# Kernel tuning notes

Hardware: AMD Instinct MI355X
Metric: run time of the kernel (lower is better)

The kernel has to match this reference:

```python
import jax, jax.numpy as jnp
import numpy as np

N_HEAD = 12
HEAD_DIM = 64
EPS = 1e-6
ROPE_BASE = 10000.0


def rms_norm(x, w):
    x32 = x.astype(jnp.float32)
    var = jnp.mean(x32 * x32, axis=-1, keepdims=True)
    xn = x32 * jax.lax.rsqrt(var + EPS)
    return w * xn.astype(x.dtype)


def rotate_half(x):
    x1, x2 = jnp.split(x, 2, axis=-1)
    return jnp.concatenate((-x2, x1), axis=-1)


def rope_cos_sin(seq_len, dtype):
    inv_freq = 1.0 / (ROPE_BASE ** (jnp.arange(0, HEAD_DIM, 2, dtype=jnp.float32) / HEAD_DIM))
    pos = jnp.arange(seq_len, dtype=jnp.float32)
    freqs = pos[:, None] * inv_freq[None, :]          # [S, HEAD_DIM//2]
    emb = jnp.concatenate((freqs, freqs), axis=-1)    # [S, HEAD_DIM]
    # shape [1, 1, S, HEAD_DIM] (batch, head, seq, dim) after unsqueeze_dim=1
    return emb[None, None].astype(dtype), None  # placeholder, see below


def setup_inputs() -> dict:
    key = jax.random.key(0)
    ks = jax.random.split(key, 9)
    B, S, D, F = 1, 4096, 768, 2048
    s = 0.02
    return {
        "hidden_states": jax.random.normal(ks[0], (B, S, D), jnp.float32),
        "w_q": jax.random.normal(ks[1], (D, D), jnp.float32) * s,
        "w_k": jax.random.normal(ks[2], (D, D), jnp.float32) * s,
        "w_v": jax.random.normal(ks[3], (D, D), jnp.float32) * s,
        "w_o": jax.random.normal(ks[4], (D, D), jnp.float32) * s,
        "w_gate": jax.random.normal(ks[5], (D, F), jnp.float32) * s,
        "w_up": jax.random.normal(ks[6], (D, F), jnp.float32) * s,
        "w_down": jax.random.normal(ks[7], (F, D), jnp.float32) * s,
        "w_norm1": jnp.ones((D,), jnp.float32),
        "w_norm2": jnp.ones((D,), jnp.float32),
    }


def attention(x, w_q, w_k, w_v, w_o):
    B, S, D = x.shape
    scale = HEAD_DIM ** -0.5
    # project and split heads: [B, H, S, hd]
    q = (x @ w_q).reshape(B, S, N_HEAD, HEAD_DIM).transpose(0, 2, 1, 3)
    k = (x @ w_k).reshape(B, S, N_HEAD, HEAD_DIM).transpose(0, 2, 1, 3)
    v = (x @ w_v).reshape(B, S, N_HEAD, HEAD_DIM).transpose(0, 2, 1, 3)
    # rotary embedding (position_ids = arange(S))
    inv_freq = 1.0 / (ROPE_BASE ** (jnp.arange(0, HEAD_DIM, 2, dtype=jnp.float32) / HEAD_DIM))
    pos = jnp.arange(S, dtype=jnp.float32)
    freqs = pos[:, None] * inv_freq[None, :]
    emb = jnp.concatenate((freqs, freqs), axis=-1)          # [S, hd]
    cos = jnp.cos(emb).astype(x.dtype)[None, None]          # [1,1,S,hd]
    sin = jnp.sin(emb).astype(x.dtype)[None, None]
    q = q * cos + rotate_half(q) * sin
    k = k * cos + rotate_half(k) * sin
    # eager attention with causal mask (materialized, as in the original)
    scores = jnp.einsum("bhqd,bhkd->bhqk", q, k) * scale
    causal = jnp.triu(jnp.ones((S, S), dtype=bool), k=1)
    scores = jnp.where(causal, jnp.finfo(scores.dtype).min, scores)
    attn = jax.nn.softmax(scores.astype(jnp.float32), axis=-1).astype(q.dtype)
    out = jnp.einsum("bhqk,bhkd->bhqd", attn, v)
    out = out.transpose(0, 2, 1, 3).reshape(B, S, D)
    return out @ w_o


def reference(hidden_states, w_q, w_k, w_v, w_o, w_gate, w_up, w_down, w_norm1, w_norm2):
    x = hidden_states
    h = x + attention(rms_norm(x, w_norm1), w_q, w_k, w_v, w_o)
    y = rms_norm(h, w_norm2)
    ffn = (jax.nn.silu(y @ w_gate) * (y @ w_up)) @ w_down
    return h + ffn
```

## Files before the change

### kernel.cpp

```cpp
#include <hip/hip_runtime.h>
#include <hip/hip_bf16.h>

typedef __attribute__((ext_vector_type(8))) short s8v;
typedef __attribute__((ext_vector_type(4))) float f4v;
typedef __attribute__((ext_vector_type(16))) float f16v;
typedef __attribute__((ext_vector_type(4))) unsigned u4v;

typedef __attribute__((address_space(1))) const void as1_void;
typedef __attribute__((address_space(3))) void as3_void;

__device__ __forceinline__ void gl16(const void* g, void* l) {
  __builtin_amdgcn_global_load_lds((as1_void*)g, (as3_void*)l, 16, 0, 0);
}

__device__ __forceinline__ float b2f(int u) {
  union { float f; unsigned i; } c; c.i = ((unsigned)(u & 0xFFFF)) << 16; return c.f;
}
__device__ __forceinline__ unsigned short f2b(float f) {
  union { float f; unsigned i; } c; c.f = f;
  unsigned r = c.i + 0x7FFFu + ((c.i >> 16) & 1u);
  return (unsigned short)(r >> 16);
}
__device__ __forceinline__ unsigned pk2(float lo, float hi) {
  unsigned u;
  asm("v_cvt_pk_bf16_f32 %0, %1, %2" : "=v"(u) : "v"(lo), "v"(hi));
  return u;
}

#define MFMA16(a, b, c) __builtin_amdgcn_mfma_f32_16x16x32_bf16((a), (b), (c), 0, 0, 0)
#define MFMA32(a, b, c) __builtin_amdgcn_mfma_f32_32x32x16_bf16((a), (b), (c), 0, 0, 0)

struct Seg { const float* src; unsigned short* dst; int K; int N; int nbn; int nblocks; int mode; };
struct PrepArgs { Seg seg[9]; float* ct; float* st; const float* wn1; };

__global__ __launch_bounds__(256) void prep_k(PrepArgs a) {
  int b = blockIdx.x, si = 0;
  while (si < 8 && b >= a.seg[si].nblocks) { b -= a.seg[si].nblocks; ++si; }
  const Seg s = a.seg[si];
  const int tid = threadIdx.x;
  if (s.mode == 3) {
    const int t = b * 256 + tid;
    const int sq = t >> 5, d = t & 31;
    const float inv = powf(10000.0f, -(float)d * (1.0f / 32.0f));
    const float ang = (float)sq * inv;
    a.ct[t] = cosf(ang);
    a.st[t] = sinf(ang);
    return;
  }
  if (s.mode == 4) {
    const float* xr = s.src + (size_t)b * 768;
    float v0 = xr[tid], v1 = xr[tid + 256], v2 = xr[tid + 512];
    float ss = v0 * v0 + v1 * v1 + v2 * v2;
#pragma unroll
    for (int m = 1; m < 64; m <<= 1) ss += __shfl_xor(ss, m, 64);
    __shared__ float sred[4];
    if ((tid & 63) == 0) sred[tid >> 6] = ss;
    __syncthreads();
    const float tot = sred[0] + sred[1] + sred[2] + sred[3];
    const float rn = rsqrtf(tot * (1.0f / 768.0f) + 1e-6f);
    unsigned short* orow = s.dst + (size_t)b * 768;
    orow[tid]       = f2b(v0 * rn * a.wn1[tid]);
    orow[tid + 256] = f2b(v1 * rn * a.wn1[tid + 256]);
    orow[tid + 512] = f2b(v2 * rn * a.wn1[tid + 512]);
    return;
  }
  __shared__ float tile[32][33];
  const int tx = tid & 31, ty = tid >> 5;
  const int bn = b % s.nbn, bk = b / s.nbn;
#pragma unroll
  for (int i = 0; i < 32; i += 8)
    tile[ty + i][tx] = s.src[(size_t)(bk * 32 + ty + i) * s.N + bn * 32 + tx];
  __syncthreads();
#pragma unroll
  for (int i = 0; i < 32; i += 8) {
    int row;
    if (s.mode == 0)      row = bn * 32 + ty + i;
    else                  row = bn * 64 + (s.mode == 2 ? 32 : 0) + ty + i;
    s.dst[(size_t)row * s.K + bk * 32 + tx] = f2b(tile[tx][ty + i]);
  }
}

__global__ __launch_bounds__(256) void rmsnorm_k(const float* __restrict__ x,
    const float* __restrict__ w, unsigned short* __restrict__ out) {
  const int row = blockIdx.x, tid = threadIdx.x;
  const float* xr = x + (size_t)row * 768;
  float v0 = xr[tid], v1 = xr[tid + 256], v2 = xr[tid + 512];
  float ss = v0 * v0 + v1 * v1 + v2 * v2;
#pragma unroll
  for (int m = 1; m < 64; m <<= 1) ss += __shfl_xor(ss, m, 64);
  __shared__ float sred[4];
  if ((tid & 63) == 0) sred[tid >> 6] = ss;
  __syncthreads();
  const float tot = sred[0] + sred[1] + sred[2] + sred[3];
  const float rn = rsqrtf(tot * (1.0f / 768.0f) + 1e-6f);
  unsigned short* orow = out + (size_t)row * 768;
  orow[tid]       = f2b(v0 * rn * w[tid]);
  orow[tid + 256] = f2b(v1 * rn * w[tid + 256]);
  orow[tid + 512] = f2b(v2 * rn * w[tid + 512]);
}

template <int EPI, int BN>
__global__ __launch_bounds__(256) void gemm_bt(const unsigned short* __restrict__ A,
    const unsigned short* __restrict__ Bt, unsigned short* __restrict__ Cb,
    float* __restrict__ Cf, const float* __restrict__ R, int K, int ldc,
    const float* __restrict__ ct, const float* __restrict__ st) {
  constexpr int ABYTES = 128 * 32 * 2;
  constexpr int BBYTES = BN * 32 * 2;
  constexpr int MR = (BN == 128) ? 4 : 2;
  __shared__ unsigned short As[3 * 128 * 32];
  __shared__ unsigned short Bs[3 * BN * 32];
  const int tid = threadIdx.x;
  const int lane = tid & 63, wid = tid >> 6;
  const int wrow = (BN == 128) ? (wid >> 1) * 64 : wid * 32;
  const int wcol = (BN == 128) ? (wid & 1) * 64 : 0;
  const int l15 = lane & 15, l4 = lane >> 4;
  const int bm = blockIdx.y, bn = blockIdx.x;

  f4v acc[MR][4] = {};

  const int o0 = tid * 16, o1 = tid * 16 + 4096;
  const int r0 = o0 >> 6, c0 = o0 & 63;
  const int r1 = o1 >> 6, c1 = o1 & 63;
  const size_t ldab = (size_t)K * 2;
  const char* Abyte = (const char*)A;
  const char* Bbyte = (const char*)Bt;
  const size_t a0 = (size_t)(bm * 128 + r0) * ldab + c0;
  const size_t a1 = (size_t)(bm * 128 + r1) * ldab + c1;
  const size_t b0 = (size_t)(bn * BN + r0) * ldab + c0;
  const size_t b1 = (size_t)(bn * BN + r1) * ldab + c1;
  char* AsB = (char*)As;
  char* BsB = (char*)Bs;
  const int uoff = wid << 10;

#define STAGEK(I, SL) do { const size_t kb = (size_t)(I) * 64;                 \
    char* Aw = AsB + (SL) * ABYTES;                                            \
    char* Bw = BsB + (SL) * BBYTES;                                            \
    gl16(Abyte + a0 + kb, Aw + uoff);                                          \
    gl16(Abyte + a1 + kb, Aw + uoff + 4096);                                   \
    gl16(Bbyte + b0 + kb, Bw + uoff);                                          \
    if constexpr (BN == 128) gl16(Bbyte + b1 + kb, Bw + uoff + 4096); } while (0)

  const int NI = K >> 5;
  STAGEK(0, 0);
  STAGEK(1, 1);
  int sel = 0, nsl = 2;

  for (int i = 0; i < NI; ++i) {
    if (i < NI - 1) {
      if constexpr (BN == 128) asm volatile("s_waitcnt vmcnt(4)" ::: "memory");
      else                     asm volatile("s_waitcnt vmcnt(3)" ::: "memory");
    } else {
      asm volatile("s_waitcnt vmcnt(0)" ::: "memory");
    }
    __builtin_amdgcn_s_barrier();
    __builtin_amdgcn_sched_barrier(0);
    if (i + 2 < NI) STAGEK(i + 2, nsl);
    const char* Ar = AsB + sel * ABYTES;
    const char* Br = BsB + sel * BBYTES;
    s8v af[MR], bf[4];
#pragma unroll
    for (int m = 0; m < MR; ++m)
      af[m] = *(const s8v*)(Ar + (wrow + m * 16 + l15) * 64 + l4 * 16);
#pragma unroll
    for (int n = 0; n < 4; ++n)
      bf[n] = *(const s8v*)(Br + (wcol + n * 16 + l15) * 64 + l4 * 16);
    __builtin_amdgcn_s_setprio(1);
#pragma unroll
    for (int m = 0; m < MR; ++m)
#pragma unroll
      for (int n = 0; n < 4; ++n) acc[m][n] = MFMA16(af[m], bf[n], acc[m][n]);
    __builtin_amdgcn_s_setprio(0);
    sel = (sel == 2) ? 0 : sel + 1;
    nsl = (nsl == 2) ? 0 : nsl + 1;
  }
#undef STAGEK

  const int row0 = bm * 128 + wrow;
  const int col0 = bn * BN + wcol;

  if (EPI == 2 && bn < 12) {
#pragma unroll
    for (int m = 0; m < MR; ++m)
#pragma unroll
      for (int r = 0; r < 4; ++r) {
        const int row = row0 + m * 16 + l4 * 4 + r;
#pragma unroll
        for (int n = 0; n < 2; ++n) {
          const int d = n * 16 + l15;
          const float c  = ct[row * 32 + d];
          const float sn = st[row * 32 + d];
          const float aa = acc[m][n][r], bb = acc[m][n + 2][r];
          acc[m][n][r]     = aa * c - bb * sn;
          acc[m][n + 2][r] = bb * c + aa * sn;
        }
      }
  }
  if (EPI == 2 && bn < 6) {
    const float QSC = 0.18033688011112042f;
#pragma unroll
    for (int m = 0; m < MR; ++m)
#pragma unroll
      for (int n = 0; n < 4; ++n)
#pragma unroll
        for (int r = 0; r < 4; ++r) acc[m][n][r] *= QSC;
  }

  if (EPI == 3) {
    const int wcx = wcol >> 6;
    const int colb = (bn * 2 + wcx) * 32;
#pragma unroll
    for (int m = 0; m < MR; ++m)
#pragma unroll
      for (int n = 0; n < 2; ++n)
#pragma unroll
        for (int r = 0; r < 4; ++r) {
          const int row = row0 + m * 16 + l4 * 4 + r;
          const float g = acc[m][n][r], u = acc[m][n + 2][r];
          const float val = g * u / (1.0f + __expf(-g));
          Cb[(size_t)row * 2048 + colb + n * 16 + l15] = f2b(val);
        }
    return;
  }

#pragma unroll
  for (int m = 0; m < MR; ++m)
#pragma unroll
    for (int n = 0; n < 4; ++n)
#pragma unroll
      for (int r = 0; r < 4; ++r) {
        const int row = row0 + m * 16 + l4 * 4 + r;
        const int col = col0 + n * 16 + l15;
        const float v = acc[m][n][r];
        if (EPI == 1) {
          Cf[(size_t)row * ldc + col] = v + R[(size_t)row * ldc + col];
        } else {
          Cb[(size_t)row * ldc + col] = f2b(v);
        }
      }
}

__global__ __launch_bounds__(256, 4) void flash_k(const unsigned short* __restrict__ qkv,
    uint2* __restrict__ Opart, float* __restrict__ ml) {
  const int kh = blockIdx.x, p = blockIdx.y, h = blockIdx.z;
  const int qbA = 63 - p;
  const int tid = threadIdx.x;
  const int wv = tid >> 6, lane = tid & 63;
  const int l31 = lane & 31, h8 = lane >> 5;
  const int myqb = (wv & 1) ? p : qbA;
  const int qrel = (wv >> 1) * 32 + l31;
  const int q_abs = myqb * 64 + qrel;

  __shared__ unsigned short Ks[2][64 * 72];
  __shared__ unsigned short Vt[2][64 * 72];

  const unsigned short* qp = qkv + h * 64;
  const unsigned short* kp = qkv + 768 + h * 64;
  const unsigned short* vp = qkv + 1536 + h * 64;

  s8v qf[4];
#pragma unroll
  for (int cc = 0; cc < 4; ++cc)
    qf[cc] = *(const s8v*)(qp + (size_t)q_abs * 2304 + cc * 16 + h8 * 8);

  f16v o0 = {}, o1 = {};
  float lp = 0.f;

  const int krow = tid >> 3, kc = (tid & 7) * 8;
  const int vj = tid & 31, vd0 = (tid >> 5) * 8;

  s8v ka, kb, va, vb;
#define LOADT(T) do { const size_t k0n = (size_t)(T) * 64;                    \
    ka = *(const s8v*)(kp + (k0n + krow) * 2304 + kc);                        \
    kb = *(const s8v*)(kp + (k0n + krow + 32) * 2304 + kc);                   \
    va = *(const s8v*)(vp + (k0n + 2 * vj) * 2304 + vd0);                     \
    vb = *(const s8v*)(vp + (k0n + 2 * vj + 1) * 2304 + vd0); } while (0)
#define WRITET(BUF) do {                                                      \
    *(s8v*)(Ks[BUF] + krow * 72 + kc) = ka;                                   \
    *(s8v*)(Ks[BUF] + (krow + 32) * 72 + kc) = kb;                            \
    unsigned* vtw = (unsigned*)(Vt[BUF] + (size_t)vd0 * 72 + 2 * vj);         \
    _Pragma("unroll")                                                         \
    for (int i = 0; i < 8; ++i)                                               \
      vtw[i * 36] = ((unsigned)(unsigned short)va[i]) |                       \
                    (((unsigned)(unsigned short)vb[i]) << 16); } while (0)

  LOADT(kh);
  WRITET(0);
  if (kh + 2 <= qbA) LOADT(kh + 2);
  __syncthreads();

  for (int t = kh; t <= qbA; t += 2) {
    const int cur = (t >> 1) & 1;
    if (t <= myqb) {
      f16v s0 = {}, s1 = {};
      __builtin_amdgcn_s_setprio(1);
#pragma unroll
      for (int cc = 0; cc < 4; ++cc) {
        const s8v kf0 = *(const s8v*)(Ks[cur] + l31 * 72 + cc * 16 + h8 * 8);
        const s8v kf1 = *(const s8v*)(Ks[cur] + (32 + l31) * 72 + cc * 16 + h8 * 8);
        s0 = MFMA32(kf0, qf[cc], s0);
        s1 = MFMA32(kf1, qf[cc], s1);
      }
      __builtin_amdgcn_s_setprio(0);
      if (t == myqb) {
#pragma unroll
        for (int rr = 0; rr < 16; ++rr) {
          const int koff = (rr & 3) + 8 * (rr >> 2) + 4 * h8;
          if (koff > qrel) s0[rr] = -1e30f;
          if (koff + 32 > qrel) s1[rr] = -1e30f;
        }
      }
#pragma unroll
      for (int rr = 0; rr < 16; ++rr) {
        s0[rr] = exp2f(s0[rr]);
        s1[rr] = exp2f(s1[rr]);
      }
      float sm[8];
#pragma unroll
      for (int i = 0; i < 8; ++i) sm[i] = (s0[i] + s0[i + 8]) + (s1[i] + s1[i + 8]);
#pragma unroll
      for (int i = 0; i < 4; ++i) sm[i] += sm[i + 4];
      lp += (sm[0] + sm[1]) + (sm[2] + sm[3]);

      unsigned pk0[8], pk1[8];
#pragma unroll
      for (int g = 0; g < 4; ++g)
#pragma unroll
        for (int j = 0; j < 2; ++j) {
          pk0[g * 2 + j] = pk2(s0[g * 4 + 2 * j], s0[g * 4 + 2 * j + 1]);
          pk1[g * 2 + j] = pk2(s1[g * 4 + 2 * j], s1[g * 4 + 2 * j + 1]);
        }
      __builtin_amdgcn_s_setprio(1);
#pragma unroll
      for (int cc = 0; cc < 4; ++cc) {
        const int g0 = (cc & 1) * 2, g1 = g0 + 1;
        const unsigned pA0 = (cc & 2) ? pk1[g0 * 2 + 0] : pk0[g0 * 2 + 0];
        const unsigned pA1 = (cc & 2) ? pk1[g0 * 2 + 1] : pk0[g0 * 2 + 1];
        const unsigned pB0 = (cc & 2) ? pk1[g1 * 2 + 0] : pk0[g1 * 2 + 0];
        const unsigned pB1 = (cc & 2) ? pk1[g1 * 2 + 1] : pk0[g1 * 2 + 1];
        const unsigned t00 = __shfl_xor((int)pA0, 32);
        const unsigned t01 = __shfl_xor((int)pA1, 32);
        const unsigned t10 = __shfl_xor((int)pB0, 32);
        const unsigned t11 = __shfl_xor((int)pB1, 32);
        union { u4v u; s8v s; } pf;
        pf.u[0] = h8 ? t10 : pA0;
        pf.u[1] = h8 ? t11 : pA1;
        pf.u[2] = h8 ? pB0 : t00;
        pf.u[3] = h8 ? pB1 : t01;
        const s8v vf0 = *(const s8v*)(Vt[cur] + l31 * 72 + cc * 16 + h8 * 8);
        const s8v vf1 = *(const s8v*)(Vt[cur] + (32 + l31) * 72 + cc * 16 + h8 * 8);
        o0 = MFMA32(vf0, pf.s, o0);
        o1 = MFMA32(vf1, pf.s, o1);
      }
      __builtin_amdgcn_s_setprio(0);
    }
    if (t + 2 <= qbA) {
      WRITET(cur ^ 1);
      if (t + 4 <= qbA) LOADT(t + 4);
      __syncthreads();
    }
  }

  lp += __shfl_xor(lp, 32);

  const size_t obase = ((size_t)kh * 12 + h) * 16 * 4096;
#pragma unroll
  for (int g = 0; g < 4; ++g) {
    const uint2 v0 = make_uint2(pk2(o0[g * 4], o0[g * 4 + 1]), pk2(o0[g * 4 + 2], o0[g * 4 + 3]));
    const uint2 v1 = make_uint2(pk2(o1[g * 4], o1[g * 4 + 1]), pk2(o1[g * 4 + 2], o1[g * 4 + 3]));
    Opart[obase + (size_t)(2 * g + h8) * 4096 + q_abs] = v0;
    Opart[obase + (size_t)(8 + 2 * g + h8) * 4096 + q_abs] = v1;
  }
  if (h8 == 0)
    ml[((size_t)kh * 12 + h) * 4096 + q_abs] = lp;
#undef LOADT
#undef WRITET
}

__global__ __launch_bounds__(256) void combine_k(const uint2* __restrict__ Opart,
    const float* __restrict__ ml, unsigned short* __restrict__ out) {
  const int u = blockIdx.x * 256 + threadIdx.x;
  const int q = u & 4095;
  const int rest = u >> 12;
  const int dgrp = rest & 15;
  const int h = rest >> 4;
  const float l0 = ml[h * 4096 + q];
  const float l1 = ml[12 * 4096 + h * 4096 + q];
  const float inv = 1.0f / (l0 + l1);
  const size_t idx = ((size_t)h * 16 + dgrp) * 4096 + q;
  const uint2 a = Opart[idx];
  const uint2 b = Opart[(size_t)12 * 16 * 4096 + idx];
  const int dbase = (dgrp < 8) ? 4 * dgrp : 32 + 4 * (dgrp - 8);
  ushort4 r;
  r.x = f2b((b2f(a.x) + b2f(b.x)) * inv);
  r.y = f2b((b2f(a.x >> 16) + b2f(b.x >> 16)) * inv);
  r.z = f2b((b2f(a.y) + b2f(b.y)) * inv);
  r.w = f2b((b2f(a.y >> 16) + b2f(b.y >> 16)) * inv);
  *(ushort4*)(out + (size_t)q * 768 + h * 64 + dbase) = r;
}

extern "C" void kernel_launch(void* const* d_in, const int* in_sizes, int n_in,
                              void* d_out, int out_size, void* d_ws, size_t ws_size,
                              hipStream_t stream) {
  const float* x    = (const float*)d_in[0];
  const float* w_q  = (const float*)d_in[1];
  const float* w_k  = (const float*)d_in[2];
  const float* w_v  = (const float*)d_in[3];
  const float* w_o  = (const float*)d_in[4];
  const float* w_g  = (const float*)d_in[5];
  const float* w_u  = (const float*)d_in[6];
  const float* w_d  = (const float*)d_in[7];
  const float* w_n1 = (const float*)d_in[8];
  const float* w_n2 = (const float*)d_in[9];
  (void)in_sizes; (void)n_in; (void)out_size; (void)ws_size;

  char* ws = (char*)d_ws;
  size_t off = 0;
  auto alloc = [&](size_t bytes) { char* p = ws + off; off += (bytes + 255) & ~(size_t)255; return p; };
  unsigned short* wqkvT = (unsigned short*)alloc(2304ull * 768 * 2);
  unsigned short* woT   = (unsigned short*)alloc(768ull * 768 * 2);
  unsigned short* wguT  = (unsigned short*)alloc(4096ull * 768 * 2);
  unsigned short* wdT   = (unsigned short*)alloc(768ull * 2048 * 2);
  float* ct             = (float*)alloc(4096ull * 32 * 4);
  float* st             = (float*)alloc(4096ull * 32 * 4);
  unsigned short* xn    = (unsigned short*)alloc(4096ull * 768 * 2);
  unsigned short* qkv   = (unsigned short*)alloc(4096ull * 2304 * 2);
  unsigned short* attn  = (unsigned short*)alloc(4096ull * 768 * 2);
  float* hbuf           = (float*)alloc(4096ull * 768 * 4);
  unsigned short* ybuf  = (unsigned short*)alloc(4096ull * 768 * 2);
  unsigned short* ffn   = (unsigned short*)alloc(4096ull * 2048 * 2);
  uint2* Opart          = (uint2*)alloc(2ull * 12 * 16 * 4096 * 8);
  float* mlb            = (float*)alloc(2ull * 12 * 4096 * 4);

  PrepArgs pa;
  pa.seg[0] = { w_q, wqkvT,                 768,  768, 24,  576, 0 };
  pa.seg[1] = { w_k, wqkvT + 768 * 768,     768,  768, 24,  576, 0 };
  pa.seg[2] = { w_v, wqkvT + 2 * 768 * 768, 768,  768, 24,  576, 0 };
  pa.seg[3] = { w_o, woT,                   768,  768, 24,  576, 0 };
  pa.seg[4] = { w_g, wguT,                  768, 2048, 64, 1536, 1 };
  pa.seg[5] = { w_u, wguT,                  768, 2048, 64, 1536, 2 };
  pa.seg[6] = { w_d, wdT,                  2048,  768, 24, 1536, 0 };
  pa.seg[7] = { nullptr, nullptr, 0, 0, 0, 512, 3 };
  pa.seg[8] = { x, xn, 0, 0, 0, 4096, 4 };
  pa.ct = ct; pa.st = st; pa.wn1 = w_n1;
  const int prep_blocks = 576 * 4 + 1536 * 3 + 512 + 4096;

  prep_k<<<prep_blocks, 256, 0, stream>>>(pa);
  gemm_bt<2, 128><<<dim3(18, 32), 256, 0, stream>>>(xn, wqkvT, qkv, nullptr, nullptr, 768, 2304, ct, st);
  flash_k<<<dim3(2, 32, 12), 256, 0, stream>>>(qkv, Opart, mlb);
  combine_k<<<3072, 256, 0, stream>>>(Opart, mlb, attn);
  gemm_bt<1, 64><<<dim3(12, 32), 256, 0, stream>>>(attn, woT, nullptr, hbuf, x, 768, 768, nullptr, nullptr);
  rmsnorm_k<<<4096, 256, 0, stream>>>(hbuf, w_n2, ybuf);
  gemm_bt<3, 128><<<dim3(32, 32), 256, 0, stream>>>(ybuf, wguT, ffn, nullptr, nullptr, 768, 2048, nullptr, nullptr);
  gemm_bt<1, 64><<<dim3(12, 32), 256, 0, stream>>>(ffn, wdT, nullptr, (float*)d_out, hbuf, 2048, 768, nullptr, nullptr);
}
```

Baseline: 222.0 us.

## Add 256x128-tile 512-thread GEMM kernel for QKV and gate/up projections

```diff
diff --git a/kernel.cpp b/kernel.cpp
--- a/kernel.cpp
+++ b/kernel.cpp
@@ -178,50 +178,6 @@
   const int row0 = bm * 128 + wrow;
   const int col0 = bn * BN + wcol;
 
-  if (EPI == 2 && bn < 12) {
-#pragma unroll
-    for (int m = 0; m < MR; ++m)
-#pragma unroll
-      for (int r = 0; r < 4; ++r) {
-        const int row = row0 + m * 16 + l4 * 4 + r;
-#pragma unroll
-        for (int n = 0; n < 2; ++n) {
-          const int d = n * 16 + l15;
-          const float c  = ct[row * 32 + d];
-          const float sn = st[row * 32 + d];
-          const float aa = acc[m][n][r], bb = acc[m][n + 2][r];
-          acc[m][n][r]     = aa * c - bb * sn;
-          acc[m][n + 2][r] = bb * c + aa * sn;
-        }
-      }
-  }
-  if (EPI == 2 && bn < 6) {
-    const float QSC = 0.18033688011112042f;
-#pragma unroll
-    for (int m = 0; m < MR; ++m)
-#pragma unroll
-      for (int n = 0; n < 4; ++n)
-#pragma unroll
-        for (int r = 0; r < 4; ++r) acc[m][n][r] *= QSC;
-  }
-
-  if (EPI == 3) {
-    const int wcx = wcol >> 6;
-    const int colb = (bn * 2 + wcx) * 32;
-#pragma unroll
-    for (int m = 0; m < MR; ++m)
-#pragma unroll
-      for (int n = 0; n < 2; ++n)
-#pragma unroll
-        for (int r = 0; r < 4; ++r) {
-          const int row = row0 + m * 16 + l4 * 4 + r;
-          const float g = acc[m][n][r], u = acc[m][n + 2][r];
-          const float val = g * u / (1.0f + __expf(-g));
-          Cb[(size_t)row * 2048 + colb + n * 16 + l15] = f2b(val);
-        }
-    return;
-  }
-
 #pragma unroll
   for (int m = 0; m < MR; ++m)
 #pragma unroll
@@ -236,6 +192,128 @@
         } else {
           Cb[(size_t)row * ldc + col] = f2b(v);
         }
+      }
+}
+
+template <int EPI>
+__global__ __launch_bounds__(512, 2) void gemm_big(const unsigned short* __restrict__ A,
+    const unsigned short* __restrict__ Bt, unsigned short* __restrict__ Cb,
+    int K, int ldc, const float* __restrict__ ct, const float* __restrict__ st) {
+  constexpr int ABYTES = 256 * 32 * 2;
+  constexpr int BBYTES = 128 * 32 * 2;
+  __shared__ unsigned short As[3 * 256 * 32];
+  __shared__ unsigned short Bs[3 * 128 * 32];
+  const int tid = threadIdx.x;
+  const int lane = tid & 63, wid = tid >> 6;
+  const int wm = wid >> 1, wn = wid & 1;
+  const int wrow = wm * 64, wcol = wn * 64;
+  const int l15 = lane & 15, l4 = lane >> 4;
+  const int bm = blockIdx.y, bn = blockIdx.x;
+
+  f4v acc[4][4] = {};
+
+  const size_t ldab = (size_t)K * 2;
+  const char* Ab = (const char*)A;
+  const char* Bb = (const char*)Bt;
+  const int lrow = lane >> 2, lch = (lane & 3) * 16;
+  const size_t aS0 = (size_t)(bm * 256 + wid * 16 + lrow) * ldab + lch;
+  const size_t aS1 = (size_t)(bm * 256 + (wid + 8) * 16 + lrow) * ldab + lch;
+  const size_t bS  = (size_t)(bn * 128 + wid * 16 + lrow) * ldab + lch;
+  char* AsB = (char*)As;
+  char* BsB = (char*)Bs;
+  const int uA0 = wid << 10, uA1 = (wid + 8) << 10, uB = wid << 10;
+
+#define STAGEK(I, SL) do { const size_t kb = (size_t)(I) * 64;                 \
+    gl16(Ab + aS0 + kb, AsB + (SL) * ABYTES + uA0);                            \
+    gl16(Ab + aS1 + kb, AsB + (SL) * ABYTES + uA1);                            \
+    gl16(Bb + bS  + kb, BsB + (SL) * BBYTES + uB); } while (0)
+
+  const int NI = K >> 5;
+  STAGEK(0, 0);
+  STAGEK(1, 1);
+  int sel = 0, nsl = 2;
+
+  for (int i = 0; i < NI; ++i) {
+    if (i < NI - 1) asm volatile("s_waitcnt vmcnt(3)" ::: "memory");
+    else            asm volatile("s_waitcnt vmcnt(0)" ::: "memory");
+    __builtin_amdgcn_s_barrier();
+    __builtin_amdgcn_sched_barrier(0);
+    if (i + 2 < NI) STAGEK(i + 2, nsl);
+    const char* Ar = AsB + sel * ABYTES;
+    const char* Br = BsB + sel * BBYTES;
+    s8v af[4], bf[4];
+#pragma unroll
+    for (int m = 0; m < 4; ++m)
+      af[m] = *(const s8v*)(Ar + (wrow + m * 16 + l15) * 64 + l4 * 16);
+#pragma unroll
+    for (int n = 0; n < 4; ++n)
+      bf[n] = *(const s8v*)(Br + (wcol + n * 16 + l15) * 64 + l4 * 16);
+    __builtin_amdgcn_s_setprio(1);
+#pragma unroll
+    for (int m = 0; m < 4; ++m)
+#pragma unroll
+      for (int n = 0; n < 4; ++n) acc[m][n] = MFMA16(af[m], bf[n], acc[m][n]);
+    __builtin_amdgcn_s_setprio(0);
+    sel = (sel == 2) ? 0 : sel + 1;
+    nsl = (nsl == 2) ? 0 : nsl + 1;
+  }
+#undef STAGEK
+
+  const int row0 = bm * 256 + wrow;
+  const int col0 = bn * 128 + wcol;
+
+  if (EPI == 2 && bn < 12) {
+#pragma unroll
+    for (int m = 0; m < 4; ++m)
+#pragma unroll
+      for (int r = 0; r < 4; ++r) {
+        const int row = row0 + m * 16 + l4 * 4 + r;
+#pragma unroll
+        for (int n = 0; n < 2; ++n) {
+          const int d = n * 16 + l15;
+          const float c  = ct[row * 32 + d];
+          const float sn = st[row * 32 + d];
+          const float aa = acc[m][n][r], bb = acc[m][n + 2][r];
+          acc[m][n][r]     = aa * c - bb * sn;
+          acc[m][n + 2][r] = bb * c + aa * sn;
+        }
+      }
+  }
+  if (EPI == 2 && bn < 6) {
+    const float QSC = 0.18033688011112042f;
+#pragma unroll
+    for (int m = 0; m < 4; ++m)
+#pragma unroll
+      for (int n = 0; n < 4; ++n)
+#pragma unroll
+        for (int r = 0; r < 4; ++r) acc[m][n][r] *= QSC;
+  }
+
+  if (EPI == 3) {
+    const int colb = (bn * 2 + wn) * 32;
+#pragma unroll
+    for (int m = 0; m < 4; ++m)
+#pragma unroll
+      for (int n = 0; n < 2; ++n)
+#pragma unroll
+        for (int r = 0; r < 4; ++r) {
+          const int row = row0 + m * 16 + l4 * 4 + r;
+          const float g = acc[m][n][r], u = acc[m][n + 2][r];
+          const float val = g * u / (1.0f + __expf(-g));
+          Cb[(size_t)row * 2048 + colb + n * 16 + l15] = f2b(val);
+        }
+    return;
+  }
+
+#pragma unroll
+  for (int m = 0; m < 4; ++m)
+#pragma unroll
+    for (int n = 0; n < 4; ++n)
+#pragma unroll
+      for (int r = 0; r < 4; ++r) {
+        const int row = row0 + m * 16 + l4 * 4 + r;
+        const int col = col0 + n * 16 + l15;
+        Cb[(size_t)row * ldc + col] = f2b(acc[m][n][r]);
       }
 }
 
@@ -445,11 +523,11 @@
   const int prep_blocks = 576 * 4 + 1536 * 3 + 512 + 4096;
 
   prep_k<<<prep_blocks, 256, 0, stream>>>(pa);
-  gemm_bt<2, 128><<<dim3(18, 32), 256, 0, stream>>>(xn, wqkvT, qkv, nullptr, nullptr, 768, 2304, ct, st);
+  gemm_big<2><<<dim3(18, 16), 512, 0, stream>>>(xn, wqkvT, qkv, 768, 2304, ct, st);
   flash_k<<<dim3(2, 32, 12), 256, 0, stream>>>(qkv, Opart, mlb);
   combine_k<<<3072, 256, 0, stream>>>(Opart, mlb, attn);
   gemm_bt<1, 64><<<dim3(12, 32), 256, 0, stream>>>(attn, woT, nullptr, hbuf, x, 768, 768, nullptr, nullptr);
   rmsnorm_k<<<4096, 256, 0, stream>>>(hbuf, w_n2, ybuf);
-  gemm_bt<3, 128><<<dim3(32, 32), 256, 0, stream>>>(ybuf, wguT, ffn, nullptr, nullptr, 768, 2048, nullptr, nullptr);
+  gemm_big<3><<<dim3(32, 16), 512, 0, stream>>>(ybuf, wguT, ffn, 768, 2048, nullptr, nullptr);
   gemm_bt<1, 64><<<dim3(12, 32), 256, 0, stream>>>(ffn, wdT, nullptr, (float*)d_out, hbuf, 2048, 768, nullptr, nullptr);
 }
```

After: 216.2 us. 1.03x faster.
